# Performance work log

Hardware: AMD Instinct MI355X
Metric: run time of the kernel (lower is better)

Reference implementation:

```python
import jax, jax.numpy as jnp
import numpy as np

WEIGHT = 0.1
SELF_WEIGHT = 1.0
OTHER_WEIGHT = 1.0

def setup_inputs() -> dict:
    key = jax.random.key(0)
    k1, k2 = jax.random.split(key)
    B, D = 8192, 128
    output = jax.random.normal(k1, (B, D), dtype=jnp.float32)
    target = jax.random.normal(k2, (B, D), dtype=jnp.float32)
    return {"output": output, "target": target}

def reference(output, target):
    # Pairwise Euclidean distances d[i, n] = ||output[i] - target[n]||_2
    # no [B, B, D] intermediate).
    B = output.shape[0]
    xx = jnp.sum(output * output, axis=-1)          # [B]
    yy = jnp.sum(target * target, axis=-1)          # [B]
    d2 = xx[:, None] + yy[None, :] - 2.0 * (output @ target.T)  # [B, B]
    d = jnp.sqrt(jnp.maximum(d2, 0.0))
    diag_sum = jnp.trace(d)                          # sum of self distances
    total_sum = jnp.sum(d)
    other_sum = total_sum - diag_sum
    loss = (-diag_sum * SELF_WEIGHT + other_sum * OTHER_WEIGHT) / B * WEIGHT
    return loss
```

## Files before the change

kernel.cpp:

```cpp
#include <hip/hip_runtime.h>
#include <stdint.h>

typedef __bf16 bf16;
typedef __bf16 bf16x8 __attribute__((ext_vector_type(8)));
typedef float f32x16 __attribute__((ext_vector_type(16)));

#define BDIM 8192
#define DDIM 128

__device__ __forceinline__ uint32_t f2bf1(float f) {
    uint32_t u = __float_as_uint(f);
    return (u + 0x7FFFu + ((u >> 16) & 1u)) >> 16;
}

__device__ __forceinline__ void gload16(const void* g, void* l) {
    __builtin_amdgcn_global_load_lds(
        (const __attribute__((address_space(1))) uint32_t*)g,
        (__attribute__((address_space(3))) uint32_t*)l,
        16, 0, 0);
}

__global__ __launch_bounds__(256) void prep_kernel(const float* __restrict__ out_f,
                                                   const float* __restrict__ tgt_f,
                                                   uint32_t* __restrict__ ab,
                                                   float* __restrict__ xxyy) {
    const float* src = blockIdx.y ? tgt_f : out_f;
    uint32_t* dst = ab + (size_t)blockIdx.y * (BDIM * DDIM / 2);
    float* nrm = xxyy + (size_t)blockIdx.y * BDIM;

    int wid = threadIdx.x >> 6;
    int lane = threadIdx.x & 63;
    int row = blockIdx.x * 4 + wid;

    const float2* s = (const float2*)(src + (size_t)row * DDIM);
    float2 v = s[lane];
    dst[row * (DDIM / 2) + lane] = f2bf1(v.x) | (f2bf1(v.y) << 16);

    float sq = v.x * v.x + v.y * v.y;
    #pragma unroll
    for (int off = 32; off > 0; off >>= 1) sq += __shfl_down(sq, off);
    if (lane == 0) nrm[row] = sq;
}

__global__ __launch_bounds__(256) void dist_kernel(const uint32_t* __restrict__ Ag,
                                                   const uint32_t* __restrict__ Bg,
                                                   const float* __restrict__ xxg,
                                                   const float* __restrict__ yyg,
                                                   float* __restrict__ partials) {
    __shared__ bf16 Al[128 * 64];
    __shared__ bf16 Bl[128 * 64];
    __shared__ float xxl[128];
    __shared__ float yyl[128];
    __shared__ float wsum[4];

    const int tid = threadIdx.x;
    const int lane = tid & 63;
    const int wid = tid >> 6;
    const int wr = wid >> 1, wc = wid & 1;
    const int bx = blockIdx.x, by = blockIdx.y;

    if (tid < 128) xxl[tid] = xxg[bx * 128 + tid];
    else           yyl[tid - 128] = yyg[by * 128 + (tid - 128)];

    const int rl = tid >> 3;
    const int g  = (tid & 7) ^ (rl & 7);
    const uint8_t* Abase = (const uint8_t*)Ag + ((size_t)bx * 128) * 256
                         + rl * 256 + g * 16;
    const uint8_t* Bbase = (const uint8_t*)Bg + ((size_t)by * 128) * 256
                         + rl * 256 + g * 16;
    uint8_t* la = (uint8_t*)Al + tid * 16;
    uint8_t* lb = (uint8_t*)Bl + tid * 16;

    const int lm = lane & 31;
    const int fh = lane >> 5;

    f32x16 acc[2][2] = {};

    #pragma unroll
    for (int ch = 0; ch < 2; ++ch) {
        if (ch) __syncthreads();
        const uint8_t* ga = Abase + ch * 128;
        const uint8_t* gb = Bbase + ch * 128;
        #pragma unroll
        for (int i = 0; i < 4; ++i) {
            gload16(ga + i * 8192, la + i * 4096);
            gload16(gb + i * 8192, lb + i * 4096);
        }
        __syncthreads();

        #pragma unroll
        for (int k0 = 0; k0 < 64; k0 += 16) {
            const int gf = (k0 >> 3) + fh;
            bf16x8 af[2], bfr[2];
            #pragma unroll
            for (int t = 0; t < 2; ++t) {
                int am = wr * 64 + t * 32 + lm;
                af[t]  = *(const bf16x8*)&Al[(am * 8 + (gf ^ (am & 7))) * 8];
                int bn = wc * 64 + t * 32 + lm;
                bfr[t] = *(const bf16x8*)&Bl[(bn * 8 + (gf ^ (bn & 7))) * 8];
            }
            acc[0][0] = __builtin_amdgcn_mfma_f32_32x32x16_bf16(af[0], bfr[0], acc[0][0], 0, 0, 0);
            acc[0][1] = __builtin_amdgcn_mfma_f32_32x32x16_bf16(af[0], bfr[1], acc[0][1], 0, 0, 0);
            acc[1][0] = __builtin_amdgcn_mfma_f32_32x32x16_bf16(af[1], bfr[0], acc[1][0], 0, 0, 0);
            acc[1][1] = __builtin_amdgcn_mfma_f32_32x32x16_bf16(af[1], bfr[1], acc[1][1], 0, 0, 0);
        }
    }

    float s = 0.0f;
    #pragma unroll
    for (int tr = 0; tr < 2; ++tr) {
        float xv[16];
        #pragma unroll
        for (int r = 0; r < 16; ++r) {
            int ml = wr * 64 + tr * 32 + (r & 3) + 8 * (r >> 2) + 4 * fh;
            xv[r] = xxl[ml];
        }
        #pragma unroll
        for (int tc = 0; tc < 2; ++tc) {
            float yv = yyl[wc * 64 + tc * 32 + lm];
            #pragma unroll
            for (int r = 0; r < 16; ++r) {
                float d2 = fmaf(-2.0f, acc[tr][tc][r], xv[r] + yv);
                s += __builtin_amdgcn_sqrtf(fmaxf(d2, 0.0f));
            }
        }
    }

    if (bx == by && wr == wc) {
        #pragma unroll
        for (int t = 0; t < 2; ++t) {
            #pragma unroll
            for (int r = 0; r < 16; ++r) {
                int row = (r & 3) + 8 * (r >> 2) + 4 * fh;
                if (row == lm) {
                    int idx = wr * 64 + t * 32 + row;
                    float d2 = fmaf(-2.0f, acc[t][t][r], xxl[idx] + yyl[idx]);
                    s -= 2.0f * __builtin_amdgcn_sqrtf(fmaxf(d2, 0.0f));
                }
            }
        }
    }

    #pragma unroll
    for (int off = 32; off > 0; off >>= 1) s += __shfl_down(s, off);
    if (lane == 0) wsum[wid] = s;
    __syncthreads();
    if (tid == 0) partials[by * 64 + bx] = wsum[0] + wsum[1] + wsum[2] + wsum[3];
}

__global__ __launch_bounds__(256) void reduce_kernel(const float* __restrict__ partials,
                                                     float* __restrict__ out) {
    __shared__ float wsum[4];
    float s = 0.0f;
    for (int i = threadIdx.x; i < 4096; i += 256) s += partials[i];
    #pragma unroll
    for (int off = 32; off > 0; off >>= 1) s += __shfl_down(s, off);
    int lane = threadIdx.x & 63, wid = threadIdx.x >> 6;
    if (lane == 0) wsum[wid] = s;
    __syncthreads();
    if (threadIdx.x == 0)
        out[0] = (wsum[0] + wsum[1] + wsum[2] + wsum[3]) * (0.1f / 8192.0f);
}

extern "C" void kernel_launch(void* const* d_in, const int* in_sizes, int n_in,
                              void* d_out, int out_size, void* d_ws, size_t ws_size,
                              hipStream_t stream) {
    const float* output = (const float*)d_in[0];
    const float* target = (const float*)d_in[1];

    uint8_t* ws = (uint8_t*)d_ws;
    uint32_t* ab      = (uint32_t*)ws;
    float*    xxyy    = (float*)(ws + 4u * 1024u * 1024u);
    float*    partial = (float*)(ws + 4u * 1024u * 1024u + 64u * 1024u);

    prep_kernel<<<dim3(2048, 2), 256, 0, stream>>>(output, target, ab, xxyy);
    dist_kernel<<<dim3(64, 64), 256, 0, stream>>>(ab, ab + (BDIM * DDIM / 2),
                                                  xxyy, xxyy + BDIM, partial);
    reduce_kernel<<<1, 256, 0, stream>>>(partial, (float*)d_out);
}
```

Before: 95.02 us.

## Switch distance GEMM from bf16 to fp8 with k-major packed layout

Operands are quantized to fp8 instead of bf16, and the prep kernel writes them in a k-chunk-major layout (16 chunks of 8 bytes per row) so the dist kernel fills LDS in one load pass with a single barrier and reads 8-byte fragments without swizzling. The MFMA switches to the fp8 32x32x16 variant, which halves operand bytes and LDS use. The epilogue splits the sqrt accumulation across two partial sums, and launch bounds request more resident blocks. The risk is precision: fp8 e4m3 quantization of the dot products adds much more error to d2 than bf16, which may go beyond the tolerance on the loss.

```diff
diff --git a/kernel.cpp b/kernel.cpp
--- a/kernel.cpp
+++ b/kernel.cpp
@@ -1,17 +1,9 @@
 #include <hip/hip_runtime.h>
 #include <stdint.h>
 
-typedef __bf16 bf16;
-typedef __bf16 bf16x8 __attribute__((ext_vector_type(8)));
 typedef float f32x16 __attribute__((ext_vector_type(16)));
 
 #define BDIM 8192
-#define DDIM 128
-
-__device__ __forceinline__ uint32_t f2bf1(float f) {
-    uint32_t u = __float_as_uint(f);
-    return (u + 0x7FFFu + ((u >> 16) & 1u)) >> 16;
-}
 
 __device__ __forceinline__ void gload16(const void* g, void* l) {
     __builtin_amdgcn_global_load_lds(
@@ -22,33 +14,41 @@
 
 __global__ __launch_bounds__(256) void prep_kernel(const float* __restrict__ out_f,
                                                    const float* __restrict__ tgt_f,
-                                                   uint32_t* __restrict__ ab,
+                                                   uint8_t* __restrict__ ak,
                                                    float* __restrict__ xxyy) {
     const float* src = blockIdx.y ? tgt_f : out_f;
-    uint32_t* dst = ab + (size_t)blockIdx.y * (BDIM * DDIM / 2);
+    uint8_t* dst = ak + (size_t)blockIdx.y * (1u << 20);
     float* nrm = xxyy + (size_t)blockIdx.y * BDIM;
 
-    int wid = threadIdx.x >> 6;
-    int lane = threadIdx.x & 63;
-    int row = blockIdx.x * 4 + wid;
+    const int tid = threadIdx.x;
+    const int lane = tid & 63;
+    const int w = tid >> 6;
+    const int j = lane & 15;
+    const int r = blockIdx.x * 16 + w * 4 + (lane >> 4);
 
-    const float2* s = (const float2*)(src + (size_t)row * DDIM);
-    float2 v = s[lane];
-    dst[row * (DDIM / 2) + lane] = f2bf1(v.x) | (f2bf1(v.y) << 16);
+    const float4* s4 = (const float4*)(src + (size_t)r * 128 + j * 8);
+    float4 a = s4[0], b = s4[1];
 
-    float sq = v.x * v.x + v.y * v.y;
-    #pragma unroll
-    for (int off = 32; off > 0; off >>= 1) sq += __shfl_down(sq, off);
-    if (lane == 0) nrm[row] = sq;
+    uint32_t w0 = __builtin_amdgcn_cvt_pk_fp8_f32(a.x, a.y, 0, false);
+    w0 = __builtin_amdgcn_cvt_pk_fp8_f32(a.z, a.w, w0, true);
+    uint32_t w1 = __builtin_amdgcn_cvt_pk_fp8_f32(b.x, b.y, 0, false);
+    w1 = __builtin_amdgcn_cvt_pk_fp8_f32(b.z, b.w, w1, true);
+    *(uint2*)(dst + j * 65536 + r * 8) = make_uint2(w0, w1);
+
+    float sq = a.x*a.x + a.y*a.y + a.z*a.z + a.w*a.w
+             + b.x*b.x + b.y*b.y + b.z*b.z + b.w*b.w;
+    sq += __shfl_xor(sq, 1); sq += __shfl_xor(sq, 2);
+    sq += __shfl_xor(sq, 4); sq += __shfl_xor(sq, 8);
+    if (j == 0) nrm[r] = sq;
 }
 
-__global__ __launch_bounds__(256) void dist_kernel(const uint32_t* __restrict__ Ag,
-                                                   const uint32_t* __restrict__ Bg,
-                                                   const float* __restrict__ xxg,
-                                                   const float* __restrict__ yyg,
-                                                   float* __restrict__ partials) {
-    __shared__ bf16 Al[128 * 64];
-    __shared__ bf16 Bl[128 * 64];
+__global__ __launch_bounds__(256, 4) void dist_kernel(const uint8_t* __restrict__ Ak,
+                                                      const uint8_t* __restrict__ Bk,
+                                                      const float* __restrict__ xxg,
+                                                      const float* __restrict__ yyg,
+                                                      float* __restrict__ partials) {
+    __shared__ uint8_t Al[16384];
+    __shared__ uint8_t Bl[16384];
     __shared__ float xxl[128];
     __shared__ float yyl[128];
     __shared__ float wsum[4];
@@ -62,51 +62,38 @@
     if (tid < 128) xxl[tid] = xxg[bx * 128 + tid];
     else           yyl[tid - 128] = yyg[by * 128 + (tid - 128)];
 
-    const int rl = tid >> 3;
-    const int g  = (tid & 7) ^ (rl & 7);
-    const uint8_t* Abase = (const uint8_t*)Ag + ((size_t)bx * 128) * 256
-                         + rl * 256 + g * 16;
-    const uint8_t* Bbase = (const uint8_t*)Bg + ((size_t)by * 128) * 256
-                         + rl * 256 + g * 16;
-    uint8_t* la = (uint8_t*)Al + tid * 16;
-    uint8_t* lb = (uint8_t*)Bl + tid * 16;
+    {
+        const uint8_t* ga = Ak + wid * 65536 + bx * 1024 + lane * 16;
+        const uint8_t* gb = Bk + wid * 65536 + by * 1024 + lane * 16;
+        uint8_t* la = Al + tid * 16;
+        uint8_t* lb = Bl + tid * 16;
+        #pragma unroll
+        for (int i = 0; i < 4; ++i) {
+            gload16(ga + i * 262144, la + i * 4096);
+            gload16(gb + i * 262144, lb + i * 4096);
+        }
+    }
+    __syncthreads();
 
     const int lm = lane & 31;
     const int fh = lane >> 5;
+    const uint8_t* abase = Al + fh * 1024 + (wr * 64 + lm) * 8;
+    const uint8_t* bbase = Bl + fh * 1024 + (wc * 64 + lm) * 8;
 
     f32x16 acc[2][2] = {};
-
     #pragma unroll
-    for (int ch = 0; ch < 2; ++ch) {
-        if (ch) __syncthreads();
-        const uint8_t* ga = Abase + ch * 128;
-        const uint8_t* gb = Bbase + ch * 128;
-        #pragma unroll
-        for (int i = 0; i < 4; ++i) {
-            gload16(ga + i * 8192, la + i * 4096);
-            gload16(gb + i * 8192, lb + i * 4096);
-        }
-        __syncthreads();
-
-        #pragma unroll
-        for (int k0 = 0; k0 < 64; k0 += 16) {
-            const int gf = (k0 >> 3) + fh;
-            bf16x8 af[2], bfr[2];
-            #pragma unroll
-            for (int t = 0; t < 2; ++t) {
-                int am = wr * 64 + t * 32 + lm;
-                af[t]  = *(const bf16x8*)&Al[(am * 8 + (gf ^ (am & 7))) * 8];
-                int bn = wc * 64 + t * 32 + lm;
-                bfr[t] = *(const bf16x8*)&Bl[(bn * 8 + (gf ^ (bn & 7))) * 8];
-            }
-            acc[0][0] = __builtin_amdgcn_mfma_f32_32x32x16_bf16(af[0], bfr[0], acc[0][0], 0, 0, 0);
-            acc[0][1] = __builtin_amdgcn_mfma_f32_32x32x16_bf16(af[0], bfr[1], acc[0][1], 0, 0, 0);
-            acc[1][0] = __builtin_amdgcn_mfma_f32_32x32x16_bf16(af[1], bfr[0], acc[1][0], 0, 0, 0);
-            acc[1][1] = __builtin_amdgcn_mfma_f32_32x32x16_bf16(af[1], bfr[1], acc[1][1], 0, 0, 0);
-        }
+    for (int s = 0; s < 8; ++s) {
+        long a0 = *(const long*)(abase + s * 2048);
+        long a1 = *(const long*)(abase + s * 2048 + 256);
+        long b0 = *(const long*)(bbase + s * 2048);
+        long b1 = *(const long*)(bbase + s * 2048 + 256);
+        acc[0][0] = __builtin_amdgcn_mfma_f32_32x32x16_fp8_fp8(a0, b0, acc[0][0], 0, 0, 0);
+        acc[0][1] = __builtin_amdgcn_mfma_f32_32x32x16_fp8_fp8(a0, b1, acc[0][1], 0, 0, 0);
+        acc[1][0] = __builtin_amdgcn_mfma_f32_32x32x16_fp8_fp8(a1, b0, acc[1][0], 0, 0, 0);
+        acc[1][1] = __builtin_amdgcn_mfma_f32_32x32x16_fp8_fp8(a1, b1, acc[1][1], 0, 0, 0);
     }
 
-    float s = 0.0f;
+    float s0 = 0.0f, s1 = 0.0f;
     #pragma unroll
     for (int tr = 0; tr < 2; ++tr) {
         float xv[16];
@@ -121,10 +108,12 @@
             #pragma unroll
             for (int r = 0; r < 16; ++r) {
                 float d2 = fmaf(-2.0f, acc[tr][tc][r], xv[r] + yv);
-                s += __builtin_amdgcn_sqrtf(fmaxf(d2, 0.0f));
+                float d = __builtin_amdgcn_sqrtf(fmaxf(d2, 0.0f));
+                if (r & 1) s1 += d; else s0 += d;
             }
         }
     }
+    float s = s0 + s1;
 
     if (bx == by && wr == wc) {
         #pragma unroll
@@ -169,12 +158,12 @@
     const float* target = (const float*)d_in[1];
 
     uint8_t* ws = (uint8_t*)d_ws;
-    uint32_t* ab      = (uint32_t*)ws;
-    float*    xxyy    = (float*)(ws + 4u * 1024u * 1024u);
-    float*    partial = (float*)(ws + 4u * 1024u * 1024u + 64u * 1024u);
+    uint8_t* ak      = ws;
+    float*   xxyy    = (float*)(ws + 2u * 1024u * 1024u);
+    float*   partial = (float*)(ws + 2u * 1024u * 1024u + 64u * 1024u);
 
-    prep_kernel<<<dim3(2048, 2), 256, 0, stream>>>(output, target, ab, xxyy);
-    dist_kernel<<<dim3(64, 64), 256, 0, stream>>>(ab, ab + (BDIM * DDIM / 2),
+    prep_kernel<<<dim3(512, 2), 256, 0, stream>>>(output, target, ak, xxyy);
+    dist_kernel<<<dim3(64, 64), 256, 0, stream>>>(ak, ak + (1u << 20),
                                                   xxyy, xxyy + BDIM, partial);
     reduce_kernel<<<1, 256, 0, stream>>>(partial, (float*)d_out);
 }
```

Result: faster. 84.16 us (-11.4%).
